# Kernel tuning notes

Hardware: AMD Instinct MI355X
Metric: run time of the kernel (lower is better)

Reference implementation:

```python
import jax, jax.numpy as jnp
import numpy as np

DIM = 256
KEY_DIM = 16
NUM_HEADS = 8
ATTN_RATIO = 4
NH_KD = KEY_DIM * NUM_HEADS   # 128
D = ATTN_RATIO * KEY_DIM      # 64
DH = D * NUM_HEADS            # 512
POS_LEN = 16
SCALE = KEY_DIM ** -0.5


def _cbn(x, w, s, b):
    # 1x1 conv (no bias) + folded BatchNorm affine. w: [out,in], x: [B,in,H,W]
    y = jnp.einsum('oi,bihw->bohw', w, x)
    return y * s[None, :, None, None] + b[None, :, None, None]


def _interp_pos(pos, n):
    # F.interpolate(mode='linear', align_corners=False) from length POS_LEN to n.
    L = pos.shape[-1]
    coords = (jnp.arange(n, dtype=pos.dtype) + 0.5) * (L / n) - 0.5
    coords = jnp.clip(coords, 0.0, L - 1)
    lo = jnp.floor(coords).astype(jnp.int32)
    hi = jnp.minimum(lo + 1, L - 1)
    t = coords - lo.astype(pos.dtype)
    return pos[..., lo] * (1 - t) + pos[..., hi] * t  # [1,C,n]


def _axial_attn(q_emb, k_emb, v_emb, pos_q, pos_k, n):
    # q_emb/k_emb: [B,NH_KD,n], v_emb: [B,DH,n]
    B = q_emb.shape[0]
    q = (q_emb + _interp_pos(pos_q, n)).reshape(B, NUM_HEADS, KEY_DIM, n)
    k = (k_emb + _interp_pos(pos_k, n)).reshape(B, NUM_HEADS, KEY_DIM, n)
    v = v_emb.reshape(B, NUM_HEADS, D, n)
    attn = jnp.einsum('bhcn,bhcm->bhnm', q, k) * SCALE
    attn = jax.nn.softmax(attn, axis=-1)
    xx = jnp.einsum('bhnm,bhdm->bhnd', attn, v)      # [B,NH,n,D]
    return xx.transpose(0, 1, 3, 2).reshape(B, DH, n)  # [B,DH,n]


def _forward(x, wq, sq, bq, wk, sk, bk, wv, sv, bv,
             pos_rowq, pos_rowk, pos_colq, pos_colk,
             w_row, s_row, b_row, w_col, s_col, b_col,
             w_proj, s_proj, b_proj, w_sc, s_sc, b_sc,
             w_dw, s_dw, b_dw, w_pw, s_pw, b_pw):
    B, C, H, W = x.shape
    q = _cbn(x, wq, sq, bq)   # [B,NH_KD,H,W]
    k = _cbn(x, wk, sk, bk)
    v = _cbn(x, wv, sv, bv)   # [B,DH,H,W]

    # row branch (mean over W)
    xx_row = _axial_attn(q.mean(-1), k.mean(-1), v.mean(-1), pos_rowq, pos_rowk, H)
    xx_row = _cbn(jax.nn.relu(xx_row[..., None]), w_row, s_row, b_row)      # [B,DH,H,1]
    # column branch (mean over H)
    xx_col = _axial_attn(q.mean(-2), k.mean(-2), v.mean(-2), pos_colq, pos_colk, W)
    xx_col = _cbn(jax.nn.relu(xx_col[:, :, None, :]), w_col, s_col, b_col)  # [B,DH,1,W]

    attn_out = v + (xx_row + xx_col)
    attn_out = _cbn(jax.nn.relu(attn_out), w_proj, s_proj, b_proj)          # [B,DIM,H,W]

    # gate branch: 1x1 -> dw3x3 -> relu -> 1x1 -> h_sigmoid
    gate = _cbn(x, w_sc, s_sc, b_sc)
    gate = jax.lax.conv_general_dilated(
        gate, w_dw, (1, 1), 'SAME',
        dimension_numbers=('NCHW', 'OIHW', 'NCHW'), feature_group_count=DIM)
    gate = gate * s_dw[None, :, None, None] + b_dw[None, :, None, None]
    gate = jax.nn.relu(gate)
    gate = _cbn(gate, w_pw, s_pw, b_pw)
    gate = jnp.clip(gate + 3.0, 0.0, 6.0) / 6.0  # h_sigmoid
    return gate * attn_out


def setup_inputs() -> dict:
    key = jax.random.key(0)
    ks = jax.random.split(key, 32)
    B, H, W = 16, 64, 64
    nrm = lambda k, sh, sc=0.05: jax.random.normal(k, sh, dtype=jnp.float32) * sc
    inp = {
        'x': nrm(ks[0], (B, DIM, H, W), 1.0),
        'wq': nrm(ks[1], (NH_KD, DIM)), 'sq': 1.0 + nrm(ks[2], (NH_KD,)), 'bq': nrm(ks[3], (NH_KD,)),
        'wk': nrm(ks[4], (NH_KD, DIM)), 'sk': 1.0 + nrm(ks[5], (NH_KD,)), 'bk': nrm(ks[6], (NH_KD,)),
        'wv': nrm(ks[7], (DH, DIM)), 'sv': 1.0 + nrm(ks[8], (DH,)), 'bv': nrm(ks[9], (DH,)),
        'pos_rowq': nrm(ks[10], (1, NH_KD, POS_LEN), 1.0), 'pos_rowk': nrm(ks[11], (1, NH_KD, POS_LEN), 1.0),
        'pos_colq': nrm(ks[12], (1, NH_KD, POS_LEN), 1.0), 'pos_colk': nrm(ks[13], (1, NH_KD, POS_LEN), 1.0),
        'w_row': nrm(ks[14], (DH, DH)), 's_row': 1.0 + nrm(ks[15], (DH,)), 'b_row': nrm(ks[16], (DH,)),
        'w_col': nrm(ks[17], (DH, DH)), 's_col': 1.0 + nrm(ks[18], (DH,)), 'b_col': nrm(ks[19], (DH,)),
        'w_proj': nrm(ks[20], (DIM, DH)), 's_proj': 1.0 + nrm(ks[21], (DIM,)), 'b_proj': nrm(ks[22], (DIM,)),
        'w_sc': nrm(ks[23], (DIM, DIM)), 's_sc': 1.0 + nrm(ks[24], (DIM,)), 'b_sc': nrm(ks[25], (DIM,)),
        'w_dw': nrm(ks[26], (DIM, 1, 3, 3)), 's_dw': 1.0 + nrm(ks[27], (DIM,)), 'b_dw': nrm(ks[28], (DIM,)),
        'w_pw': nrm(ks[29], (DIM, DIM)), 's_pw': 1.0 + nrm(ks[30], (DIM,)), 'b_pw': nrm(ks[31], (DIM,)),
    }
    return inp


def reference(x, wq, sq, bq, wk, sk, bk, wv, sv, bv,
              pos_rowq, pos_rowk, pos_colq, pos_colk,
              w_row, s_row, b_row, w_col, s_col, b_col,
              w_proj, s_proj, b_proj, w_sc, s_sc, b_sc,
              w_dw, s_dw, b_dw, w_pw, s_pw, b_pw):
    return _forward(x, wq, sq, bq, wk, sk, bk, wv, sv, bv,
                    pos_rowq, pos_rowk, pos_colq, pos_colk,
                    w_row, s_row, b_row, w_col, s_col, b_col,
                    w_proj, s_proj, b_proj, w_sc, s_sc, b_sc,
                    w_dw, s_dw, b_dw, w_pw, s_pw, b_pw)
```

## Files before the change

kernel.cpp:

```cpp
#include <hip/hip_runtime.h>
#include <math.h>

typedef unsigned short u16;
typedef unsigned int u32;
typedef short short8 __attribute__((ext_vector_type(8)));
typedef float f32x4 __attribute__((ext_vector_type(4)));

#define Bn 16
#define Cc 256
#define Pp 4096
#define DHc 512
#define PTOT 65536
#define SCALE 0.25f

__device__ __forceinline__ float bf2f(u16 u) {
    return __uint_as_float(((u32)u) << 16);
}
__device__ __forceinline__ u16 f2bf(float f) {
    u32 u = __float_as_uint(f);
    u32 lsb = (u >> 16) & 1u;
    u += 0x7fffu + lsb;
    return (u16)(u >> 16);
}

__device__ __forceinline__ void gload16(const u16* g, u16* l) {
    __builtin_amdgcn_global_load_lds(
        (const __attribute__((address_space(1))) void*)(uintptr_t)g,
        (__attribute__((address_space(3))) void*)(u32)(uintptr_t)l,
        16, 0, 0);
}

__global__ __launch_bounds__(256) void mean_kernel(
    const float* __restrict__ x, u16* __restrict__ xmb) {
    __shared__ float plane[64][65];
    int bc = blockIdx.x;
    int b = bc >> 8, c = bc & 255;
    const float* xp = x + (size_t)bc * Pp;
    int tid = threadIdx.x;
#pragma unroll
    for (int k = 0; k < 16; ++k) {
        int idx = tid + k * 256;
        plane[idx >> 6][idx & 63] = xp[idx];
    }
    __syncthreads();
    if (tid < 64) {
        float s = 0.f;
#pragma unroll
        for (int w = 0; w < 64; ++w) s += plane[tid][w];
        xmb[((size_t)b * 64 + tid) * 256 + c] = f2bf(s * (1.f / 64.f));
    } else if (tid < 128) {
        int w = tid - 64;
        float s = 0.f;
#pragma unroll
        for (int h = 0; h < 64; ++h) s += plane[h][w];
        xmb[((size_t)1024 + b * 64 + w) * 256 + c] = f2bf(s * (1.f / 64.f));
    }
}

__global__ __launch_bounds__(256) void xpose_kernel(
    const float* __restrict__ x, u16* __restrict__ xbf) {
    __shared__ float tile[64][65];
    int pb = blockIdx.x;
    int cb = blockIdx.y;
    int b = blockIdx.z;
    int t = threadIdx.x;
    int p_l = t & 63, c_q = t >> 6;
    const float* xp = x + ((size_t)b * Cc + cb * 64) * Pp + pb * 64;
#pragma unroll
    for (int rr = 0; rr < 16; ++rr) {
        int c_l = rr * 4 + c_q;
        tile[p_l][c_l] = xp[(size_t)c_l * Pp + p_l];
    }
    __syncthreads();
    int c_l2 = t & 63, p_q = t >> 6;
    u16* dst = xbf + ((size_t)b * Pp + pb * 64) * Cc + cb * 64;
#pragma unroll
    for (int rr = 0; rr < 16; ++rr) {
        int p_l2 = rr * 4 + p_q;
        dst[(size_t)p_l2 * Cc + c_l2] = f2bf(tile[p_l2][c_l2]);
    }
}

__global__ __launch_bounds__(256) void wconv_kernel(
    const float* __restrict__ wq, const float* __restrict__ wk, const float* __restrict__ wv,
    const float* __restrict__ wsc, const float* __restrict__ wproj, const float* __restrict__ wpw,
    const float* __restrict__ wrow, const float* __restrict__ wcol,
    const float* __restrict__ wdw,
    u16* __restrict__ wqkvb, u16* __restrict__ wscb,
    u16* __restrict__ wprojb, u16* __restrict__ wpwb,
    u16* __restrict__ wrb, u16* __restrict__ wcb, float* __restrict__ wdwT) {
    int t = blockIdx.x * 256 + threadIdx.x;
    if (t < 2304) wdwT[(t % 9) * 256 + (t / 9)] = wdw[t];
    if (t < 32768) wqkvb[t] = f2bf(wq[t]);
    else if (t < 65536) wqkvb[t] = f2bf(wk[t - 32768]);
    else if (t < 196608) wqkvb[t] = f2bf(wv[t - 65536]);
    else if (t < 262144) wscb[t - 196608] = f2bf(wsc[t - 196608]);
    else if (t < 393216) wprojb[t - 262144] = f2bf(wproj[t - 262144]);
    else if (t < 458752) wpwb[t - 393216] = f2bf(wpw[t - 393216]);
    else if (t < 720896) wrb[t - 458752] = f2bf(wrow[t - 458752]);
    else wcb[t - 720896] = f2bf(wcol[t - 720896]);
}

__device__ __forceinline__ void gemm_mainloop(
    const u16* __restrict__ W, const u16* __restrict__ X, int K,
    int o0, size_t prow0, u16* ldsA, u16* ldsB, f32x4 (&acc)[4][4]) {
    int t = threadIdx.x;
    int w = t >> 6, lane = t & 63;
    int sr = (w << 5) + (lane >> 2);
    int ks = (lane & 3) * 8;
    const u16* gA = W + (size_t)(o0 + sr) * K + ks;
    const u16* gB = X + (prow0 + sr) * K + ks;
    u16* lA = ldsA + sr * 32 + ks;
    u16* lB = ldsB + sr * 32 + ks;
    int wo = (w >> 1) * 64, wp = (w & 1) * 64;
    const u16* fA = ldsA + (wo + (lane & 15)) * 32 + ((lane >> 4) * 8);
    const u16* fB = ldsB + (wp + (lane & 15)) * 32 + ((lane >> 4) * 8);

    for (int k0 = 0; k0 < K; k0 += 32) {
        if (k0) __syncthreads();
        gload16(gA + k0, lA);
        gload16(gA + k0 + (size_t)16 * K, lA + 16 * 32);
        gload16(gB + k0, lB);
        gload16(gB + k0 + (size_t)16 * K, lB + 16 * 32);
        __syncthreads();
        short8 a[4], b[4];
#pragma unroll
        for (int i = 0; i < 4; ++i) a[i] = *(const short8*)(fA + i * 16 * 32);
#pragma unroll
        for (int j = 0; j < 4; ++j) b[j] = *(const short8*)(fB + j * 16 * 32);
#pragma unroll
        for (int i = 0; i < 4; ++i)
#pragma unroll
            for (int j = 0; j < 4; ++j)
                acc[i][j] = __builtin_amdgcn_mfma_f32_16x16x32_bf16(a[i], b[j], acc[i][j], 0, 0, 0);
    }
}

__global__ __launch_bounds__(256) void gemm_qkv(
    const u16* __restrict__ Wb, const u16* __restrict__ X,
    const float* __restrict__ sq, const float* __restrict__ bq,
    const float* __restrict__ sk, const float* __restrict__ bk,
    const float* __restrict__ sv, const float* __restrict__ bv,
    const float* __restrict__ posrq, const float* __restrict__ posrk,
    const float* __restrict__ poscq, const float* __restrict__ posck,
    float* __restrict__ qrow, float* __restrict__ krow, float* __restrict__ vrow,
    float* __restrict__ qcol, float* __restrict__ kcol, float* __restrict__ vcol) {
    __shared__ u16 ldsA[128 * 32];
    __shared__ u16 ldsB[128 * 32];
    f32x4 acc[4][4];
#pragma unroll
    for (int i = 0; i < 4; ++i)
#pragma unroll
        for (int j = 0; j < 4; ++j) acc[i][j] = (f32x4){0.f, 0.f, 0.f, 0.f};
    int o0 = blockIdx.x * 128;
    size_t prow0 = (size_t)blockIdx.y * 128;
    gemm_mainloop(Wb, X, 256, o0, prow0, ldsA, ldsB, acc);

    int lane = threadIdx.x & 63, w = threadIdx.x >> 6;
    int wo = (w >> 1) * 64, wp = (w & 1) * 64;
    int quad = lane >> 4, cn = lane & 15;
#pragma unroll
    for (int j = 0; j < 4; ++j) {
        int p = (int)prow0 + wp + j * 16 + cn;
        int branch = p >> 10, loc = p & 1023;
        int b = loc >> 6, n = loc & 63;
        float coords = 0.25f * (float)n - 0.375f;
        coords = fminf(fmaxf(coords, 0.f), 15.f);
        int lo = (int)floorf(coords);
        int hi = min(lo + 1, 15);
        float tt = coords - (float)lo;
#pragma unroll
        for (int i = 0; i < 4; ++i) {
            int o = o0 + wo + i * 16 + quad * 4;
            if (o < 128) {
                const float* pos = branch ? poscq : posrq;
                float* dst = branch ? qcol : qrow;
#pragma unroll
                for (int r = 0; r < 4; ++r) {
                    int c = o + r;
                    float pv = pos[c * 16 + lo] * (1.f - tt) + pos[c * 16 + hi] * tt;
                    dst[b * 8192 + c * 64 + n] = acc[i][j][r] * sq[c] + bq[c] + pv;
                }
            } else if (o < 256) {
                const float* pos = branch ? posck : posrk;
                float* dst = branch ? kcol : krow;
#pragma unroll
                for (int r = 0; r < 4; ++r) {
                    int c = o - 128 + r;
                    float pv = pos[c * 16 + lo] * (1.f - tt) + pos[c * 16 + hi] * tt;
                    dst[b * 8192 + c * 64 + n] = acc[i][j][r] * sk[c] + bk[c] + pv;
                }
            } else {
                float* dst = branch ? vcol : vrow;
#pragma unroll
                for (int r = 0; r < 4; ++r) {
                    int c = o - 256 + r;
                    dst[b * 32768 + c * 64 + n] = acc[i][j][r] * sv[c] + bv[c];
                }
            }
        }
    }
}

__global__ __launch_bounds__(512) void attn_kernel(
    const float* __restrict__ qr, const float* __restrict__ kr, const float* __restrict__ vr,
    const float* __restrict__ qc, const float* __restrict__ kc, const float* __restrict__ vc,
    u16* __restrict__ xxbf) {
    int branch = blockIdx.y;
    const float* q = branch ? qc : qr;
    const float* k = branch ? kc : kr;
    const float* v = branch ? vc : vr;
    int bh = blockIdx.x;
    int b = bh >> 3, h = bh & 7;
    __shared__ float qs[16][64], ks[16][64], vs[64][64];
    int t = threadIdx.x;
#pragma unroll
    for (int i = t; i < 1024; i += 512) {
        int c = i >> 6, nn = i & 63;
        qs[c][nn] = q[b * 8192 + (h * 16 + c) * 64 + nn];
        ks[c][nn] = k[b * 8192 + (h * 16 + c) * 64 + nn];
    }
#pragma unroll
    for (int i = t; i < 4096; i += 512) {
        int d = i >> 6, nn = i & 63;
        vs[d][nn] = v[b * 32768 + (h * 64 + d) * 64 + nn];
    }
    __syncthreads();

    int n = t & 63, dq = t >> 6;
    float qv[16];
#pragma unroll
    for (int c = 0; c < 16; ++c) qv[c] = qs[c][n];

    float s[64];
    float mx = -1e30f;
    for (int m = 0; m < 64; ++m) {
        float acc = 0.f;
#pragma unroll
        for (int c = 0; c < 16; ++c) acc += qv[c] * ks[c][m];
        acc *= SCALE;
        s[m] = acc;
        mx = fmaxf(mx, acc);
    }
    float sum = 0.f;
    for (int m = 0; m < 64; ++m) {
        s[m] = __expf(s[m] - mx);
        sum += s[m];
    }
    float inv = 1.f / sum;
    u16* dst = xxbf + (((size_t)(b * 2 + branch)) * 64 + n) * 512 + h * 64 + dq * 8;
#pragma unroll
    for (int dd = 0; dd < 8; ++dd) {
        int d = dq * 8 + dd;
        float acc = 0.f;
#pragma unroll 8
        for (int m = 0; m < 64; ++m) acc += s[m] * vs[d][m];
        dst[dd] = f2bf(fmaxf(acc * inv, 0.f));
    }
}

__global__ __launch_bounds__(256) void post_gemm(
    const u16* __restrict__ xxbf, const u16* __restrict__ wrb, const u16* __restrict__ wcb,
    const float* __restrict__ s_row, const float* __restrict__ b_row,
    const float* __restrict__ s_col, const float* __restrict__ b_col,
    float* __restrict__ xr2, float* __restrict__ xc2) {
    __shared__ u16 ldsA[64 * 32];
    __shared__ u16 ldsB[256 * 32];
    int o0 = blockIdx.x * 256;
    int b = blockIdx.y;
    int branch = blockIdx.z;
    const u16* A = xxbf + ((size_t)(b * 2 + branch)) * 64 * 512;
    const u16* W = branch ? wcb : wrb;
    const float* ss = branch ? s_col : s_row;
    const float* bb = branch ? b_col : b_row;
    float* dst = (branch ? xc2 : xr2) + (size_t)b * 32768;

    f32x4 acc[4][4];
#pragma unroll
    for (int i = 0; i < 4; ++i)
#pragma unroll
        for (int j = 0; j < 4; ++j) acc[i][j] = (f32x4){0.f, 0.f, 0.f, 0.f};

    int t = threadIdx.x, w = t >> 6, lane = t & 63;
    int ks = (t & 3) * 8;
    const u16* gA = A + (size_t)(t >> 2) * 512 + ks;
    const u16* gB = W + (size_t)(o0 + (t >> 2)) * 512 + ks;
    u16* lA = ldsA + (t >> 2) * 32 + ks;
    u16* lB = ldsB + (t >> 2) * 32 + ks;
    const u16* fA = ldsA + (lane & 15) * 32 + ((lane >> 4) * 8);
    const u16* fB = ldsB + (w * 64 + (lane & 15)) * 32 + ((lane >> 4) * 8);

    for (int k0 = 0; k0 < 512; k0 += 32) {
        if (k0) __syncthreads();
        gload16(gA + k0, lA);
#pragma unroll
        for (int r = 0; r < 4; ++r)
            gload16(gB + k0 + (size_t)r * 64 * 512, lB + r * 64 * 32);
        __syncthreads();
        short8 a[4], bfr[4];
#pragma unroll
        for (int i = 0; i < 4; ++i) a[i] = *(const short8*)(fA + i * 16 * 32);
#pragma unroll
        for (int j = 0; j < 4; ++j) bfr[j] = *(const short8*)(fB + j * 16 * 32);
#pragma unroll
        for (int i = 0; i < 4; ++i)
#pragma unroll
            for (int j = 0; j < 4; ++j)
                acc[i][j] = __builtin_amdgcn_mfma_f32_16x16x32_bf16(a[i], bfr[j], acc[i][j], 0, 0, 0);
    }

    int quad = lane >> 4, cn = lane & 15;
#pragma unroll
    for (int i = 0; i < 4; ++i)
#pragma unroll
        for (int j = 0; j < 4; ++j) {
            int o = o0 + w * 64 + j * 16 + cn;
            float sv_ = ss[o], bv_ = bb[o];
#pragma unroll
            for (int r = 0; r < 4; ++r) {
                int n = i * 16 + quad * 4 + r;
                dst[n * 512 + o] = acc[i][j][r] * sv_ + bv_;
            }
        }
}

__global__ __launch_bounds__(256) void gemm_sc(
    const u16* __restrict__ Wb, const u16* __restrict__ X,
    const float* __restrict__ s, const float* __restrict__ bb, u16* __restrict__ outb) {
    __shared__ u16 ldsA[128 * 32];
    __shared__ u16 ldsB[128 * 32];
    f32x4 acc[4][4];
#pragma unroll
    for (int i = 0; i < 4; ++i)
#pragma unroll
        for (int j = 0; j < 4; ++j) acc[i][j] = (f32x4){0.f, 0.f, 0.f, 0.f};
    int o0 = blockIdx.x * 128;
    size_t prow0 = (size_t)blockIdx.y * 128;
    gemm_mainloop(Wb, X, 256, o0, prow0, ldsA, ldsB, acc);

    int lane = threadIdx.x & 63, w = threadIdx.x >> 6;
    int wo = (w >> 1) * 64, wp = (w & 1) * 64;
    int quad = lane >> 4, cn = lane & 15;
#pragma unroll
    for (int i = 0; i < 4; ++i) {
        int ob = o0 + wo + i * 16 + quad * 4;
        f32x4 s4 = *(const f32x4*)&s[ob];
        f32x4 b4 = *(const f32x4*)&bb[ob];
#pragma unroll
        for (int j = 0; j < 4; ++j) {
            size_t p = prow0 + wp + j * 16 + cn;
            ushort4 o4;
            o4.x = f2bf(acc[i][j][0] * s4[0] + b4[0]);
            o4.y = f2bf(acc[i][j][1] * s4[1] + b4[1]);
            o4.z = f2bf(acc[i][j][2] * s4[2] + b4[2]);
            o4.w = f2bf(acc[i][j][3] * s4[3] + b4[3]);
            *(ushort4*)&outb[p * 256 + ob] = o4;
        }
    }
}

__global__ __launch_bounds__(256) void gemm_v(
    const u16* __restrict__ Wb, const u16* __restrict__ X,
    const float* __restrict__ s, const float* __restrict__ bb,
    const float* __restrict__ xr2, const float* __restrict__ xc2, u16* __restrict__ outb) {
    __shared__ u16 ldsA[128 * 32];
    __shared__ u16 ldsB[128 * 32];
    f32x4 acc[4][4];
#pragma unroll
    for (int i = 0; i < 4; ++i)
#pragma unroll
        for (int j = 0; j < 4; ++j) acc[i][j] = (f32x4){0.f, 0.f, 0.f, 0.f};
    int o0 = blockIdx.x * 128;
    size_t prow0 = (size_t)blockIdx.y * 128;
    gemm_mainloop(Wb, X, 256, o0, prow0, ldsA, ldsB, acc);

    int lane = threadIdx.x & 63, w = threadIdx.x >> 6;
    int wo = (w >> 1) * 64, wp = (w & 1) * 64;
    int quad = lane >> 4, cn = lane & 15;
#pragma unroll
    for (int i = 0; i < 4; ++i) {
        int ob = o0 + wo + i * 16 + quad * 4;
        f32x4 s4 = *(const f32x4*)&s[ob];
        f32x4 b4 = *(const f32x4*)&bb[ob];
#pragma unroll
        for (int j = 0; j < 4; ++j) {
            size_t p = prow0 + wp + j * 16 + cn;
            int bi = (int)(p >> 12), hh = (int)((p >> 6) & 63), ww = (int)(p & 63);
            f32x4 ra = *(const f32x4*)&xr2[(size_t)bi * 32768 + hh * 512 + ob];
            f32x4 ca = *(const f32x4*)&xc2[(size_t)bi * 32768 + ww * 512 + ob];
            ushort4 o4;
            o4.x = f2bf(fmaxf(acc[i][j][0] * s4[0] + b4[0] + ra[0] + ca[0], 0.f));
            o4.y = f2bf(fmaxf(acc[i][j][1] * s4[1] + b4[1] + ra[1] + ca[1], 0.f));
            o4.z = f2bf(fmaxf(acc[i][j][2] * s4[2] + b4[2] + ra[2] + ca[2], 0.f));
            o4.w = f2bf(fmaxf(acc[i][j][3] * s4[3] + b4[3] + ra[3] + ca[3], 0.f));
            *(ushort4*)&outb[p * 512 + ob] = o4;
        }
    }
}

__global__ __launch_bounds__(256) void gemm_pw(
    const u16* __restrict__ Wb, const u16* __restrict__ X,
    const float* __restrict__ s, const float* __restrict__ bb, u16* __restrict__ outb) {
    __shared__ u16 ldsA[128 * 32];
    __shared__ u16 ldsB[128 * 32];
    f32x4 acc[4][4];
#pragma unroll
    for (int i = 0; i < 4; ++i)
#pragma unroll
        for (int j = 0; j < 4; ++j) acc[i][j] = (f32x4){0.f, 0.f, 0.f, 0.f};
    int o0 = blockIdx.x * 128;
    size_t prow0 = (size_t)blockIdx.y * 128;
    gemm_mainloop(Wb, X, 256, o0, prow0, ldsA, ldsB, acc);

    int lane = threadIdx.x & 63, w = threadIdx.x >> 6;
    int wo = (w >> 1) * 64, wp = (w & 1) * 64;
    int quad = lane >> 4, cn = lane & 15;
#pragma unroll
    for (int i = 0; i < 4; ++i) {
        int ob = o0 + wo + i * 16 + quad * 4;
        f32x4 s4 = *(const f32x4*)&s[ob];
        f32x4 b4 = *(const f32x4*)&bb[ob];
#pragma unroll
        for (int j = 0; j < 4; ++j) {
            size_t p = prow0 + wp + j * 16 + cn;
            ushort4 o4;
            o4.x = f2bf(fminf(fmaxf(acc[i][j][0] * s4[0] + b4[0] + 3.f, 0.f), 6.f) * (1.f / 6.f));
            o4.y = f2bf(fminf(fmaxf(acc[i][j][1] * s4[1] + b4[1] + 3.f, 0.f), 6.f) * (1.f / 6.f));
            o4.z = f2bf(fminf(fmaxf(acc[i][j][2] * s4[2] + b4[2] + 3.f, 0.f), 6.f) * (1.f / 6.f));
            o4.w = f2bf(fminf(fmaxf(acc[i][j][3] * s4[3] + b4[3] + 3.f, 0.f), 6.f) * (1.f / 6.f));
            *(ushort4*)&outb[p * 256 + ob] = o4;
        }
    }
}

__global__ __launch_bounds__(256) void gemm_proj(
    const u16* __restrict__ Wb, const u16* __restrict__ X,
    const float* __restrict__ s, const float* __restrict__ bb,
    const u16* __restrict__ gate, float* __restrict__ out) {
    __shared__ u16 ldsA[128 * 32];
    __shared__ u16 ldsB[128 * 32];
    f32x4 acc[4][4];
#pragma unroll
    for (int i = 0; i < 4; ++i)
#pragma unroll
        for (int j = 0; j < 4; ++j) acc[i][j] = (f32x4){0.f, 0.f, 0.f, 0.f};
    int o0 = blockIdx.x * 128;
    size_t prow0 = (size_t)blockIdx.y * 128;
    gemm_mainloop(Wb, X, 512, o0, prow0, ldsA, ldsB, acc);

    int lane = threadIdx.x & 63, w = threadIdx.x >> 6;
    int wo = (w >> 1) * 64, wp = (w & 1) * 64;
    int quad = lane >> 4, cn = lane & 15;
#pragma unroll
    for (int i = 0; i < 4; ++i) {
        int ob = o0 + wo + i * 16 + quad * 4;
        f32x4 s4 = *(const f32x4*)&s[ob];
        f32x4 b4 = *(const f32x4*)&bb[ob];
#pragma unroll
        for (int j = 0; j < 4; ++j) {
            size_t p = prow0 + wp + j * 16 + cn;
            int bi = (int)(p >> 12), pl = (int)(p & 4095);
            ushort4 gv = *(const ushort4*)&gate[p * 256 + ob];
            float* op = out + (size_t)bi * 1048576 + (size_t)ob * 4096 + pl;
            op[0 * 4096] = bf2f(gv.x) * (acc[i][j][0] * s4[0] + b4[0]);
            op[1 * 4096] = bf2f(gv.y) * (acc[i][j][1] * s4[1] + b4[1]);
            op[2 * 4096] = bf2f(gv.z) * (acc[i][j][2] * s4[2] + b4[2]);
            op[3 * 4096] = bf2f(gv.w) * (acc[i][j][3] * s4[3] + b4[3]);
        }
    }
}

__global__ __launch_bounds__(256) void dw_kernel(
    const u16* __restrict__ sc, const float* __restrict__ wdwT,
    const float* __restrict__ sdw, const float* __restrict__ bdw, u16* __restrict__ dwout) {
    int t = blockIdx.x * 256 + threadIdx.x;
    int cg = (t & 31) * 8;
    size_t p = (size_t)(t >> 5);
    int h = (int)((p >> 6) & 63), w_ = (int)(p & 63);
    float acc[8] = {0.f, 0.f, 0.f, 0.f, 0.f, 0.f, 0.f, 0.f};
#pragma unroll
    for (int ky = 0; ky < 3; ++ky) {
        int hh = h + ky - 1;
        if (hh < 0 || hh > 63) continue;
#pragma unroll
        for (int kx = 0; kx < 3; ++kx) {
            int wx = w_ + kx - 1;
            if (wx < 0 || wx > 63) continue;
            size_t pp = (size_t)((long long)p + (ky - 1) * 64 + (kx - 1));
            short8 v = *(const short8*)&sc[pp * 256 + cg];
            const float* wt = &wdwT[(ky * 3 + kx) * 256 + cg];
            f32x4 w0 = *(const f32x4*)wt;
            f32x4 w1 = *(const f32x4*)(wt + 4);
            acc[0] += w0[0] * bf2f((u16)v[0]); acc[1] += w0[1] * bf2f((u16)v[1]);
            acc[2] += w0[2] * bf2f((u16)v[2]); acc[3] += w0[3] * bf2f((u16)v[3]);
            acc[4] += w1[0] * bf2f((u16)v[4]); acc[5] += w1[1] * bf2f((u16)v[5]);
            acc[6] += w1[2] * bf2f((u16)v[6]); acc[7] += w1[3] * bf2f((u16)v[7]);
        }
    }
    f32x4 s0 = *(const f32x4*)&sdw[cg], s1 = *(const f32x4*)&sdw[cg + 4];
    f32x4 b0 = *(const f32x4*)&bdw[cg], b1 = *(const f32x4*)&bdw[cg + 4];
    short8 o;
    o[0] = (short)f2bf(fmaxf(acc[0] * s0[0] + b0[0], 0.f));
    o[1] = (short)f2bf(fmaxf(acc[1] * s0[1] + b0[1], 0.f));
    o[2] = (short)f2bf(fmaxf(acc[2] * s0[2] + b0[2], 0.f));
    o[3] = (short)f2bf(fmaxf(acc[3] * s0[3] + b0[3], 0.f));
    o[4] = (short)f2bf(fmaxf(acc[4] * s1[0] + b1[0], 0.f));
    o[5] = (short)f2bf(fmaxf(acc[5] * s1[1] + b1[1], 0.f));
    o[6] = (short)f2bf(fmaxf(acc[6] * s1[2] + b1[2], 0.f));
    o[7] = (short)f2bf(fmaxf(acc[7] * s1[3] + b1[3], 0.f));
    *(short8*)&dwout[p * 256 + cg] = o;
}

extern "C" void kernel_launch(void* const* d_in, const int* in_sizes, int n_in,
                              void* d_out, int out_size, void* d_ws, size_t ws_size,
                              hipStream_t stream) {
    const float* x = (const float*)d_in[0];
    const float* wq = (const float*)d_in[1];
    const float* sq = (const float*)d_in[2];
    const float* bq = (const float*)d_in[3];
    const float* wk = (const float*)d_in[4];
    const float* sk = (const float*)d_in[5];
    const float* bk = (const float*)d_in[6];
    const float* wv = (const float*)d_in[7];
    const float* sv = (const float*)d_in[8];
    const float* bv = (const float*)d_in[9];
    const float* posrq = (const float*)d_in[10];
    const float* posrk = (const float*)d_in[11];
    const float* poscq = (const float*)d_in[12];
    const float* posck = (const float*)d_in[13];
    const float* w_row = (const float*)d_in[14];
    const float* s_row = (const float*)d_in[15];
    const float* b_row = (const float*)d_in[16];
    const float* w_col = (const float*)d_in[17];
    const float* s_col = (const float*)d_in[18];
    const float* b_col = (const float*)d_in[19];
    const float* w_proj = (const float*)d_in[20];
    const float* s_proj = (const float*)d_in[21];
    const float* b_proj = (const float*)d_in[22];
    const float* w_sc = (const float*)d_in[23];
    const float* s_sc = (const float*)d_in[24];
    const float* b_sc = (const float*)d_in[25];
    const float* w_dw = (const float*)d_in[26];
    const float* s_dw = (const float*)d_in[27];
    const float* b_dw = (const float*)d_in[28];
    const float* w_pw = (const float*)d_in[29];
    const float* s_pw = (const float*)d_in[30];
    const float* b_pw = (const float*)d_in[31];
    float* out = (float*)d_out;

    float* fws = (float*)d_ws;
    float* qrow = fws;
    float* krow = qrow + 131072;
    float* qcol = krow + 131072;
    float* kcol = qcol + 131072;
    float* vrow = kcol + 131072;
    float* vcol = vrow + 524288;
    float* xr2  = vcol + 524288;
    float* xc2  = xr2 + 524288;
    float* wdwT = xc2 + 524288;
    u16* xmb    = (u16*)(wdwT + 2304);
    u16* xbf    = xmb + 524288;
    u16* wqkvb  = xbf + (size_t)PTOT * 256;
    u16* wscb   = wqkvb + 196608;
    u16* wprojb = wscb + 65536;
    u16* wpwb   = wprojb + 131072;
    u16* wrb    = wpwb + 65536;
    u16* wcb    = wrb + 262144;
    u16* xxbf   = wcb + 262144;
    u16* scb    = xxbf + 1048576;
    u16* dwb    = scb + (size_t)PTOT * 256;
    u16* abuf   = dwb + (size_t)PTOT * 256;
    u16* gate   = scb;

    mean_kernel<<<dim3(Bn * Cc), 256, 0, stream>>>(x, xmb);
    xpose_kernel<<<dim3(64, 4, Bn), 256, 0, stream>>>(x, xbf);
    wconv_kernel<<<dim3(3840), 256, 0, stream>>>(
        wq, wk, wv, w_sc, w_proj, w_pw, w_row, w_col, w_dw,
        wqkvb, wscb, wprojb, wpwb, wrb, wcb, wdwT);
    gemm_qkv<<<dim3(6, 16), 256, 0, stream>>>(
        wqkvb, xmb, sq, bq, sk, bk, sv, bv,
        posrq, posrk, poscq, posck, qrow, krow, vrow, qcol, kcol, vcol);
    attn_kernel<<<dim3(128, 2), 512, 0, stream>>>(qrow, krow, vrow, qcol, kcol, vcol, xxbf);
    post_gemm<<<dim3(2, Bn, 2), 256, 0, stream>>>(
        xxbf, wrb, wcb, s_row, b_row, s_col, b_col, xr2, xc2);
    gemm_sc<<<dim3(2, 512), 256, 0, stream>>>(wscb, xbf, s_sc, b_sc, scb);
    dw_kernel<<<dim3(8192), 256, 0, stream>>>(scb, wdwT, s_dw, b_dw, dwb);
    gemm_v<<<dim3(4, 512), 256, 0, stream>>>(wqkvb + 65536, xbf, sv, bv, xr2, xc2, abuf);
    gemm_pw<<<dim3(2, 512), 256, 0, stream>>>(wpwb, dwb, s_pw, b_pw, gate);
    gemm_proj<<<dim3(2, 512), 256, 0, stream>>>(wprojb, abuf, s_proj, b_proj, gate, out);
}
```

Before: 483.7 us.

## Fuse V projection GEMM and output projection GEMM through shared memory

Replaces the separate gemm_v and gemm_proj kernels with one kernel. Each 512-thread block computes the 512-channel activated V tile for 64 pixels and keeps it in a swizzled LDS buffer, then runs the projection GEMM from that buffer. This removes the global write and re-read of the 64K x 512 bf16 intermediate and one launch. In exchange the block uses about 100KB of LDS, which limits occupancy, and the mainloop is not pipelined. Each block also reloads both full weight matrices, so weight traffic grows.

```diff
diff --git a/kernel.cpp b/kernel.cpp
--- a/kernel.cpp
+++ b/kernel.cpp
@@ -359,45 +359,6 @@
     }
 }
 
-__global__ __launch_bounds__(256) void gemm_v(
-    const u16* __restrict__ Wb, const u16* __restrict__ X,
-    const float* __restrict__ s, const float* __restrict__ bb,
-    const float* __restrict__ xr2, const float* __restrict__ xc2, u16* __restrict__ outb) {
-    __shared__ u16 ldsA[128 * 32];
-    __shared__ u16 ldsB[128 * 32];
-    f32x4 acc[4][4];
-#pragma unroll
-    for (int i = 0; i < 4; ++i)
-#pragma unroll
-        for (int j = 0; j < 4; ++j) acc[i][j] = (f32x4){0.f, 0.f, 0.f, 0.f};
-    int o0 = blockIdx.x * 128;
-    size_t prow0 = (size_t)blockIdx.y * 128;
-    gemm_mainloop(Wb, X, 256, o0, prow0, ldsA, ldsB, acc);
-
-    int lane = threadIdx.x & 63, w = threadIdx.x >> 6;
-    int wo = (w >> 1) * 64, wp = (w & 1) * 64;
-    int quad = lane >> 4, cn = lane & 15;
-#pragma unroll
-    for (int i = 0; i < 4; ++i) {
-        int ob = o0 + wo + i * 16 + quad * 4;
-        f32x4 s4 = *(const f32x4*)&s[ob];
-        f32x4 b4 = *(const f32x4*)&bb[ob];
-#pragma unroll
-        for (int j = 0; j < 4; ++j) {
-            size_t p = prow0 + wp + j * 16 + cn;
-            int bi = (int)(p >> 12), hh = (int)((p >> 6) & 63), ww = (int)(p & 63);
-            f32x4 ra = *(const f32x4*)&xr2[(size_t)bi * 32768 + hh * 512 + ob];
-            f32x4 ca = *(const f32x4*)&xc2[(size_t)bi * 32768 + ww * 512 + ob];
-            ushort4 o4;
-            o4.x = f2bf(fmaxf(acc[i][j][0] * s4[0] + b4[0] + ra[0] + ca[0], 0.f));
-            o4.y = f2bf(fmaxf(acc[i][j][1] * s4[1] + b4[1] + ra[1] + ca[1], 0.f));
-            o4.z = f2bf(fmaxf(acc[i][j][2] * s4[2] + b4[2] + ra[2] + ca[2], 0.f));
-            o4.w = f2bf(fmaxf(acc[i][j][3] * s4[3] + b4[3] + ra[3] + ca[3], 0.f));
-            *(ushort4*)&outb[p * 512 + ob] = o4;
-        }
-    }
-}
-
 __global__ __launch_bounds__(256) void gemm_pw(
     const u16* __restrict__ Wb, const u16* __restrict__ X,
     const float* __restrict__ s, const float* __restrict__ bb, u16* __restrict__ outb) {
@@ -433,39 +394,123 @@
     }
 }
 
-__global__ __launch_bounds__(256) void gemm_proj(
-    const u16* __restrict__ Wb, const u16* __restrict__ X,
-    const float* __restrict__ s, const float* __restrict__ bb,
+__global__ __launch_bounds__(512) void fused_vproj(
+    const u16* __restrict__ Wv, const u16* __restrict__ Wp,
+    const u16* __restrict__ X,
+    const float* __restrict__ sv, const float* __restrict__ bv,
+    const float* __restrict__ xr2, const float* __restrict__ xc2,
+    const float* __restrict__ sp, const float* __restrict__ bp,
     const u16* __restrict__ gate, float* __restrict__ out) {
-    __shared__ u16 ldsA[128 * 32];
-    __shared__ u16 ldsB[128 * 32];
-    f32x4 acc[4][4];
+    __shared__ u16 abt[64 * 512];
+    __shared__ u16 ldsA[512 * 32];
+    __shared__ u16 ldsB[64 * 32];
+
+    int t = threadIdx.x;
+    int lane = t & 63, w = t >> 6;
+    int quad = lane >> 4, cn = lane & 15;
+    int p0 = blockIdx.x * 64;
+    int bi = p0 >> 12;
+    int hh = (p0 >> 6) & 63;
+
+    f32x4 acc1[4][4];
 #pragma unroll
     for (int i = 0; i < 4; ++i)
 #pragma unroll
-        for (int j = 0; j < 4; ++j) acc[i][j] = (f32x4){0.f, 0.f, 0.f, 0.f};
-    int o0 = blockIdx.x * 128;
-    size_t prow0 = (size_t)blockIdx.y * 128;
-    gemm_mainloop(Wb, X, 512, o0, prow0, ldsA, ldsB, acc);
-
-    int lane = threadIdx.x & 63, w = threadIdx.x >> 6;
-    int wo = (w >> 1) * 64, wp = (w & 1) * 64;
-    int quad = lane >> 4, cn = lane & 15;
+        for (int j = 0; j < 4; ++j) acc1[i][j] = (f32x4){0.f, 0.f, 0.f, 0.f};
+
+    int rowA = t >> 2, seg = t & 3;
+    int ow = w * 64;
+    const u16* fA = ldsA + (ow + cn) * 32 + quad * 8;
+    const u16* fB = ldsB + cn * 32 + quad * 8;
+
+    for (int k0 = 0; k0 < 256; k0 += 32) {
+        if (k0) __syncthreads();
+#pragma unroll
+        for (int kk = 0; kk < 4; ++kk)
+            gload16(Wv + (size_t)(rowA + kk * 128) * 256 + k0 + seg * 8,
+                    ldsA + ((size_t)t + kk * 512) * 8);
+        if (t < 256)
+            gload16(X + ((size_t)p0 + rowA) * 256 + k0 + seg * 8, ldsB + (size_t)t * 8);
+        __syncthreads();
+        short8 a[4], b[4];
+#pragma unroll
+        for (int i = 0; i < 4; ++i) a[i] = *(const short8*)(fA + i * 16 * 32);
+#pragma unroll
+        for (int j = 0; j < 4; ++j) b[j] = *(const short8*)(fB + j * 16 * 32);
+#pragma unroll
+        for (int i = 0; i < 4; ++i)
+#pragma unroll
+            for (int j = 0; j < 4; ++j)
+                acc1[i][j] = __builtin_amdgcn_mfma_f32_16x16x32_bf16(a[i], b[j], acc1[i][j], 0, 0, 0);
+    }
+
 #pragma unroll
     for (int i = 0; i < 4; ++i) {
-        int ob = o0 + wo + i * 16 + quad * 4;
-        f32x4 s4 = *(const f32x4*)&s[ob];
-        f32x4 b4 = *(const f32x4*)&bb[ob];
+        int ob = ow + i * 16 + quad * 4;
+        f32x4 s4 = *(const f32x4*)&sv[ob];
+        f32x4 b4 = *(const f32x4*)&bv[ob];
+        f32x4 ra = *(const f32x4*)&xr2[(size_t)bi * 32768 + hh * 512 + ob];
 #pragma unroll
         for (int j = 0; j < 4; ++j) {
-            size_t p = prow0 + wp + j * 16 + cn;
-            int bi = (int)(p >> 12), pl = (int)(p & 4095);
-            ushort4 gv = *(const ushort4*)&gate[p * 256 + ob];
-            float* op = out + (size_t)bi * 1048576 + (size_t)ob * 4096 + pl;
-            op[0 * 4096] = bf2f(gv.x) * (acc[i][j][0] * s4[0] + b4[0]);
-            op[1 * 4096] = bf2f(gv.y) * (acc[i][j][1] * s4[1] + b4[1]);
-            op[2 * 4096] = bf2f(gv.z) * (acc[i][j][2] * s4[2] + b4[2]);
-            op[3 * 4096] = bf2f(gv.w) * (acc[i][j][3] * s4[3] + b4[3]);
+            int p = j * 16 + cn;
+            f32x4 ca = *(const f32x4*)&xc2[(size_t)bi * 32768 + p * 512 + ob];
+            ushort4 o4;
+            o4.x = f2bf(fmaxf(acc1[i][j][0] * s4[0] + b4[0] + ra[0] + ca[0], 0.f));
+            o4.y = f2bf(fmaxf(acc1[i][j][1] * s4[1] + b4[1] + ra[1] + ca[1], 0.f));
+            o4.z = f2bf(fmaxf(acc1[i][j][2] * s4[2] + b4[2] + ra[2] + ca[2], 0.f));
+            o4.w = f2bf(fmaxf(acc1[i][j][3] * s4[3] + b4[3] + ra[3] + ca[3], 0.f));
+            *(ushort4*)&abt[p * 512 + (ob ^ ((p & 7) << 3))] = o4;
+        }
+    }
+    __syncthreads();
+
+    f32x4 acc2[4][2];
+#pragma unroll
+    for (int i = 0; i < 4; ++i)
+#pragma unroll
+        for (int j = 0; j < 2; ++j) acc2[i][j] = (f32x4){0.f, 0.f, 0.f, 0.f};
+
+    int o2w = (w & 3) * 64, pw = (w >> 2) * 32;
+    const u16* fA2 = ldsA + (o2w + cn) * 32 + quad * 8;
+    int kfrag = quad * 8;
+
+    for (int k0 = 0; k0 < 512; k0 += 32) {
+        if (k0) __syncthreads();
+        gload16(Wp + (size_t)rowA * 512 + k0 + seg * 8, ldsA + (size_t)t * 8);
+        gload16(Wp + ((size_t)rowA + 128) * 512 + k0 + seg * 8, ldsA + ((size_t)t + 512) * 8);
+        __syncthreads();
+        short8 a2[4], b2[2];
+#pragma unroll
+        for (int i = 0; i < 4; ++i) a2[i] = *(const short8*)(fA2 + i * 16 * 32);
+#pragma unroll
+        for (int j = 0; j < 2; ++j) {
+            int p = pw + j * 16 + cn;
+            int kk = k0 + kfrag;
+            b2[j] = *(const short8*)&abt[p * 512 + (kk ^ ((p & 7) << 3))];
+        }
+#pragma unroll
+        for (int i = 0; i < 4; ++i)
+#pragma unroll
+            for (int j = 0; j < 2; ++j)
+                acc2[i][j] = __builtin_amdgcn_mfma_f32_16x16x32_bf16(a2[i], b2[j], acc2[i][j], 0, 0, 0);
+    }
+
+    int pl = p0 & 4095;
+#pragma unroll
+    for (int i = 0; i < 4; ++i) {
+        int ob = o2w + i * 16 + quad * 4;
+        f32x4 s4 = *(const f32x4*)&sp[ob];
+        f32x4 b4 = *(const f32x4*)&bp[ob];
+#pragma unroll
+        for (int j = 0; j < 2; ++j) {
+            int p = pw + j * 16 + cn;
+            size_t pg = (size_t)p0 + p;
+            ushort4 gv = *(const ushort4*)&gate[pg * 256 + ob];
+            float* op = out + (size_t)bi * 1048576 + (size_t)ob * 4096 + (pl + p);
+            op[0 * 4096] = bf2f(gv.x) * (acc2[i][j][0] * s4[0] + b4[0]);
+            op[1 * 4096] = bf2f(gv.y) * (acc2[i][j][1] * s4[1] + b4[1]);
+            op[2 * 4096] = bf2f(gv.z) * (acc2[i][j][2] * s4[2] + b4[2]);
+            op[3 * 4096] = bf2f(gv.w) * (acc2[i][j][3] * s4[3] + b4[3]);
         }
     }
 }
@@ -569,7 +614,6 @@
     u16* xxbf   = wcb + 262144;
     u16* scb    = xxbf + 1048576;
     u16* dwb    = scb + (size_t)PTOT * 256;
-    u16* abuf   = dwb + (size_t)PTOT * 256;
     u16* gate   = scb;
 
     mean_kernel<<<dim3(Bn * Cc), 256, 0, stream>>>(x, xmb);
@@ -585,7 +629,7 @@
         xxbf, wrb, wcb, s_row, b_row, s_col, b_col, xr2, xc2);
     gemm_sc<<<dim3(2, 512), 256, 0, stream>>>(wscb, xbf, s_sc, b_sc, scb);
     dw_kernel<<<dim3(8192), 256, 0, stream>>>(scb, wdwT, s_dw, b_dw, dwb);
-    gemm_v<<<dim3(4, 512), 256, 0, stream>>>(wqkvb + 65536, xbf, sv, bv, xr2, xc2, abuf);
     gemm_pw<<<dim3(2, 512), 256, 0, stream>>>(wpwb, dwb, s_pw, b_pw, gate);
-    gemm_proj<<<dim3(2, 512), 256, 0, stream>>>(wprojb, abuf, s_proj, b_proj, gate, out);
-}
+    fused_vproj<<<dim3(1024), 512, 0, stream>>>(
+        wqkvb + 65536, wprojb, xbf, sv, bv, xr2, xc2, s_proj, b_proj, gate, out);
+}
```

Measured after the change: 459.0 us. 1.05x faster.
